# Kernel tuning notes

Hardware: AMD Instinct MI355X
Metric: run time of the kernel (lower is better)

Reference implementation:

```python
import jax, jax.numpy as jnp
import numpy as np

N = 100000   # nodes
E = 1600000  # edges
F_IN = 128
HID = 128
C = 40
EPS = 1e-5


def setup_inputs() -> dict:
    key = jax.random.key(0)
    ks = jax.random.split(key, 8)
    x = jax.random.normal(ks[0], (N, F_IN), dtype=jnp.float32)
    edge_index = jax.random.randint(ks[1], (2, E), 0, N, dtype=jnp.int32)
    s = 0.05
    return {
        "x": x,
        "edge_index": edge_index,
        "W1": jax.random.normal(ks[2], (F_IN, HID), dtype=jnp.float32) * s,
        "b1": jnp.zeros((HID,), jnp.float32),
        "g1": jnp.ones((HID,), jnp.float32),
        "be1": jnp.zeros((HID,), jnp.float32),
        "W2": jax.random.normal(ks[3], (HID, HID), dtype=jnp.float32) * s,
        "b2": jnp.zeros((HID,), jnp.float32),
        "g2": jnp.ones((HID,), jnp.float32),
        "be2": jnp.zeros((HID,), jnp.float32),
        "W3": jax.random.normal(ks[4], (HID, C), dtype=jnp.float32) * s,
        "b3": jnp.zeros((C,), jnp.float32),
    }


def _gcn_conv(x, W, b, src, dst, deg_inv_sqrt):
    # h = X W; then symmetric-normalized aggregation over edges (incl. self loops)
    h = x @ W                                  # [N, out]
    coef = deg_inv_sqrt[src] * deg_inv_sqrt[dst]  # [E+N]
    msg = h[src] * coef[:, None]               # gather + scale
    out = jax.ops.segment_sum(msg, dst, num_segments=N)
    return out + b


def _batchnorm(x, g, be):
    mean = jnp.mean(x, axis=0)
    var = jnp.mean(jnp.square(x - mean), axis=0)  # biased var (torch BN train)
    return (x - mean) * jax.lax.rsqrt(var + EPS) * g + be


def reference(x, edge_index, W1, b1, g1, be1, W2, b2, g2, be2, W3, b3):
    # add self loops once
    loop = jnp.arange(N, dtype=edge_index.dtype)
    src = jnp.concatenate([edge_index[0], loop])
    dst = jnp.concatenate([edge_index[1], loop])
    deg = jax.ops.segment_sum(jnp.ones_like(dst, dtype=x.dtype), dst, num_segments=N)
    dinv = jax.lax.rsqrt(deg)  # deg >= 1 due to self loops

    h = _gcn_conv(x, W1, b1, src, dst, dinv)
    h = _batchnorm(h, g1, be1)
    h = h + x                      # residual: hidden_dim == num_features
    h = jax.nn.relu(h)             # dropout: eval-mode identity

    h = _gcn_conv(h, W2, b2, src, dst, dinv)
    h = _batchnorm(h, g2, be2)
    h = jax.nn.relu(h)

    h = _gcn_conv(h, W3, b3, src, dst, dinv)
    return jax.nn.log_softmax(h, axis=1)
```

## Files before the change

### kernel.cpp

```cpp
#include <hip/hip_runtime.h>
#include <hip/hip_bf16.h>

#define NN 100000
#define EE 1600000
#define HID 128
#define CLS 40
#define EPSBN 1e-5f
#define NBUK ((NN + 255) >> 8)
#define CAP 6144
#define EPB 4096
#define GROWS (NN / 8)
#define FINB 500

typedef float f32x4 __attribute__((ext_vector_type(4)));
typedef float f32x2 __attribute__((ext_vector_type(2)));
typedef short s16x8 __attribute__((ext_vector_type(8)));
union U48 { uint4 u; s16x8 s; };

static __device__ __forceinline__ unsigned short f2bf(float f) {
    unsigned u = __float_as_uint(f);
    unsigned r = (u + 0x7fff + ((u >> 16) & 1)) >> 16;
    return (unsigned short)r;
}
static __device__ __forceinline__ unsigned pack2(float a, float b) {
    return (unsigned)f2bf(a) | ((unsigned)f2bf(b) << 16);
}
static __device__ __forceinline__ float bflo(unsigned v) { return __uint_as_float(v << 16); }
static __device__ __forceinline__ float bfhi(unsigned v) { return __uint_as_float(v & 0xffff0000u); }


__global__ void prep_all(const float* __restrict__ W1, const float* __restrict__ W2,
                         const float* __restrict__ W3,
                         unsigned* __restrict__ Wf1, unsigned* __restrict__ Wf2,
                         unsigned* __restrict__ Wf3,
                         int* gcur, float* stats1, float* stats2) {
    int blk = blockIdx.x;
    int tid = threadIdx.x;
    if (blk < 64) {
        const float* W = (blk < 32) ? W1 : W2;
        unsigned* Wf = (blk < 32) ? Wf1 : Wf2;
        int t = ((blk & 31) << 8) + tid;
        int q = t & 3, lane = (t >> 2) & 63, f = t >> 8;
        int ks = f >> 3, ct = f & 7;
        int k = ks * 32 + ((lane >> 4) << 3) + q * 2;
        int col = ct * 16 + (lane & 15);
        Wf[t] = pack2(W[k * 128 + col], W[(k + 1) * 128 + col]);
    } else if (blk < 76) {
        int t = ((blk - 64) << 8) + tid;
        int q = t & 3, lane = (t >> 2) & 63, f = t >> 8;
        int ks = f / 3, ct = f - ks * 3;
        int k = ks * 32 + ((lane >> 4) << 3) + q * 2;
        int col = ct * 16 + (lane & 15);
        float v0 = (col < CLS) ? W3[k * CLS + col] : 0.0f;
        float v1 = (col < CLS) ? W3[(k + 1) * CLS + col] : 0.0f;
        Wf3[t] = pack2(v0, v1);
    } else {
        int j = ((blk - 76) << 8) + tid;
        if (j < NBUK) gcur[j] = j * CAP;
        if (blk == 76) {
            stats1[tid] = 0.0f;
            stats2[tid] = 0.0f;
        }
    }
}


__global__ __launch_bounds__(256) void fill_p1_binned(const int* __restrict__ src,
                                                      const int* __restrict__ dst,
                                                      int* gcur, int* __restrict__ tmp) {
    __shared__ int cnt[NBUK];
    __shared__ int base[NBUK];
    int tid = threadIdx.x;
    for (int j = tid; j < NBUK; j += 256) cnt[j] = 0;
    __syncthreads();

    int es[16], ed[16];
    int i0 = blockIdx.x * EPB;
#pragma unroll
    for (int k = 0; k < 16; k++) {
        int i = i0 + k * 256 + tid;
        bool ok = i < EE;
        es[k] = ok ? src[i] : -1;
        ed[k] = ok ? dst[i] : 0;
        if (ok) atomicAdd(&cnt[ed[k] >> 8], 1);
    }
    __syncthreads();
    for (int j = tid; j < NBUK; j += 256) {
        int c = cnt[j];
        base[j] = c ? atomicAdd(&gcur[j], c) : 0;
        cnt[j] = 0;
    }
    __syncthreads();
#pragma unroll
    for (int k = 0; k < 16; k++) {
        if (es[k] >= 0) {
            int b = ed[k] >> 8;
            int r = atomicAdd(&cnt[b], 1);
            tmp[base[b] + r] = (es[k] << 8) | (ed[k] & 255);
        }
    }
}

__global__ __launch_bounds__(512) void bucket_scan(const int* __restrict__ gcur,
                                                   int* __restrict__ gbase,
                                                   int* __restrict__ row_ptr) {
    __shared__ int sc[512];
    int tid = threadIdx.x;
    int v = (tid < NBUK) ? gcur[tid] - tid * CAP : 0;
    sc[tid] = v;
    __syncthreads();
    for (int off = 1; off < 512; off <<= 1) {
        int t = (tid >= off) ? sc[tid - off] : 0;
        __syncthreads();
        sc[tid] += t;
        __syncthreads();
    }
    if (tid < NBUK) gbase[tid] = sc[tid] - v;
    if (tid == NBUK - 1) {
        gbase[NBUK] = sc[tid];
        row_ptr[NN] = sc[tid];
    }
}

__global__ __launch_bounds__(256) void fill_p2(const int* __restrict__ tmp,
                                               const int* __restrict__ gcur,
                                               const int* __restrict__ gbase,
                                               float* __restrict__ dinv,
                                               int* __restrict__ row_ptr,
                                               int* __restrict__ csr) {
    __shared__ int cnt[256];
    __shared__ int sc[256];
    __shared__ int cur[256];
    int b = blockIdx.x;
    int tid = threadIdx.x;
    int total = gcur[b] - b * CAP;
    cnt[tid] = 0;
    __syncthreads();
    int lo = b * CAP;
    for (int k = tid; k < total; k += 256) atomicAdd(&cnt[tmp[lo + k] & 255], 1);
    __syncthreads();
    int c = cnt[tid];
    sc[tid] = c;
    __syncthreads();
    for (int off = 1; off < 256; off <<= 1) {
        int t = (tid >= off) ? sc[tid - off] : 0;
        __syncthreads();
        sc[tid] += t;
        __syncthreads();
    }
    int node = (b << 8) + tid;
    int rp = gbase[b] + sc[tid] - c;
    if (node < NN) {
        dinv[node] = rsqrtf((float)(c + 1));
        row_ptr[node] = rp;
    }
    cur[tid] = rp;
    __syncthreads();
    for (int k = tid; k < total; k += 256) {
        int v = tmp[lo + k];
        int p = atomicAdd(&cur[v & 255], 1);
        csr[p] = ((unsigned)v) >> 8;
    }
}


#define LDA 136

template <int MODE>
__global__ __launch_bounds__(256) void gemm128_mfma(const float* __restrict__ Xf,
                                                    const unsigned* __restrict__ Xb,
                                                    const unsigned* __restrict__ Wf,
                                                    const float* __restrict__ stats,
                                                    const float* __restrict__ gam,
                                                    const float* __restrict__ bet,
                                                    const float* __restrict__ xres,
                                                    const float* __restrict__ dinv,
                                                    unsigned char* __restrict__ Hb) {
    __shared__ unsigned short As[64 * LDA];
    __shared__ float scs[128];
    __shared__ float shs[128];
    int t = threadIdx.x;
    int lane = t & 63, w = t >> 6;
    int wr = w >> 1, wc = w & 1;
    int blk_row = blockIdx.x * 64;
    const float invN = 1.0f / (float)NN;

    s16x8 b[4][4];
    const uint4* Wv = (const uint4*)Wf;
#pragma unroll
    for (int ks = 0; ks < 4; ks++)
#pragma unroll
        for (int ct = 0; ct < 4; ct++) {
            int f = ks * 8 + wc * 4 + ct;
            U48 u; u.u = Wv[f * 64 + lane];
            b[ks][ct] = u.s;
        }

    if (MODE == 1) {
        if (t < 128) {
            float mean = stats[t] * invN;
            float var = stats[128 + t] * invN - mean * mean;
            float sc = gam[t] * rsqrtf(var + EPSBN);
            scs[t] = sc;
            shs[t] = bet[t] - mean * sc;
        }
        __syncthreads();
        const uint2* H2 = (const uint2*)Xb;
        const float4* R4 = (const float4*)xres;
#pragma unroll
        for (int i = 0; i < 8; i++) {
            int idx = i * 256 + t;
            int row = idx >> 5, c4 = idx & 31;
            int grow = blk_row + row;
            uint2 h = make_uint2(0u, 0u);
            float4 r = make_float4(0, 0, 0, 0);
            if (grow < NN) {
                h = H2[(size_t)grow * 32 + c4];
                r = R4[(size_t)grow * 32 + c4];
            }
            int f0 = c4 * 4;
            float v0 = fmaxf(fmaf(bflo(h.x), scs[f0 + 0], shs[f0 + 0]) + r.x, 0.0f);
            float v1 = fmaxf(fmaf(bfhi(h.x), scs[f0 + 1], shs[f0 + 1]) + r.y, 0.0f);
            float v2 = fmaxf(fmaf(bflo(h.y), scs[f0 + 2], shs[f0 + 2]) + r.z, 0.0f);
            float v3 = fmaxf(fmaf(bfhi(h.y), scs[f0 + 3], shs[f0 + 3]) + r.w, 0.0f);
            *(uint2*)&As[row * LDA + c4 * 4] = make_uint2(pack2(v0, v1), pack2(v2, v3));
        }
    } else {
        const float4* X4 = (const float4*)Xf;
#pragma unroll
        for (int i = 0; i < 8; i++) {
            int idx = i * 256 + t;
            int row = idx >> 5, c4 = idx & 31;
            int grow = blk_row + row;
            float4 a = make_float4(0, 0, 0, 0);
            if (grow < NN) a = X4[(size_t)grow * 32 + c4];
            *(uint2*)&As[row * LDA + c4 * 4] = make_uint2(pack2(a.x, a.y), pack2(a.z, a.w));
        }
    }
    __syncthreads();

    f32x4 acc[2][4] = {};
    int lrow = lane & 15;
    int koff = (lane >> 4) << 3;

#pragma unroll
    for (int ks = 0; ks < 4; ks++) {
        int k0 = ks * 32 + koff;
#pragma unroll
        for (int rf = 0; rf < 2; rf++) {
            int rloc = wr * 32 + rf * 16 + lrow;
            U48 a;
            a.u = *(const uint4*)&As[rloc * LDA + k0];
#pragma unroll
            for (int ct = 0; ct < 4; ct++)
                acc[rf][ct] = __builtin_amdgcn_mfma_f32_16x16x32_bf16(a.s, b[ks][ct], acc[rf][ct], 0, 0, 0);
        }
    }

#pragma unroll
    for (int rf = 0; rf < 2; rf++) {
        int rbase = blk_row + wr * 32 + rf * 16 + ((lane >> 4) << 2);
        float dv[4];
#pragma unroll
        for (int r = 0; r < 4; r++) dv[r] = (rbase + r < NN) ? dinv[rbase + r] : 0.0f;
#pragma unroll
        for (int ct = 0; ct < 4; ct++) {
            int col = wc * 64 + ct * 16 + lrow;
#pragma unroll
            for (int r = 0; r < 4; r++) {
                int row = rbase + r;
                if (row < NN) {
                    int pv = __builtin_amdgcn_cvt_pk_fp8_f32(acc[rf][ct][r] * dv[r], 0.0f, 0, false);
                    Hb[(size_t)row * 128 + col] = (unsigned char)pv;
                }
            }
        }
    }
}

__global__ __launch_bounds__(256) void gemm40_mfma(const unsigned* __restrict__ Xb,
                                                   const unsigned* __restrict__ Wf,
                                                   const float* __restrict__ stats,
                                                   const float* __restrict__ gam,
                                                   const float* __restrict__ bet,
                                                   const float* __restrict__ dinv,
                                                   unsigned char* __restrict__ H3) {
    __shared__ unsigned short As[64 * LDA];
    __shared__ float scs[128];
    __shared__ float shs[128];
    int t = threadIdx.x;
    int lane = t & 63, w = t >> 6;
    int blk_row = blockIdx.x * 64;
    const float invN = 1.0f / (float)NN;

    s16x8 b[4][3];
    const uint4* Wv = (const uint4*)Wf;
#pragma unroll
    for (int ks = 0; ks < 4; ks++)
#pragma unroll
        for (int ct = 0; ct < 3; ct++) {
            U48 u; u.u = Wv[(ks * 3 + ct) * 64 + lane];
            b[ks][ct] = u.s;
        }

    if (t < 128) {
        float mean = stats[t] * invN;
        float var = stats[128 + t] * invN - mean * mean;
        float sc = gam[t] * rsqrtf(var + EPSBN);
        scs[t] = sc;
        shs[t] = bet[t] - mean * sc;
    }
    __syncthreads();
    const uint2* H2 = (const uint2*)Xb;
#pragma unroll
    for (int i = 0; i < 8; i++) {
        int idx = i * 256 + t;
        int row = idx >> 5, c4 = idx & 31;
        int grow = blk_row + row;
        uint2 h = make_uint2(0u, 0u);
        if (grow < NN) h = H2[(size_t)grow * 32 + c4];
        int f0 = c4 * 4;
        float v0 = fmaxf(fmaf(bflo(h.x), scs[f0 + 0], shs[f0 + 0]), 0.0f);
        float v1 = fmaxf(fmaf(bfhi(h.x), scs[f0 + 1], shs[f0 + 1]), 0.0f);
        float v2 = fmaxf(fmaf(bflo(h.y), scs[f0 + 2], shs[f0 + 2]), 0.0f);
        float v3 = fmaxf(fmaf(bfhi(h.y), scs[f0 + 3], shs[f0 + 3]), 0.0f);
        *(uint2*)&As[row * LDA + c4 * 4] = make_uint2(pack2(v0, v1), pack2(v2, v3));
    }
    __syncthreads();

    f32x4 acc[3] = {};
    int lrow = lane & 15;
    int koff = (lane >> 4) << 3;

#pragma unroll
    for (int ks = 0; ks < 4; ks++) {
        int k0 = ks * 32 + koff;
        int rloc = w * 16 + lrow;
        U48 a;
        a.u = *(const uint4*)&As[rloc * LDA + k0];
#pragma unroll
        for (int ct = 0; ct < 3; ct++)
            acc[ct] = __builtin_amdgcn_mfma_f32_16x16x32_bf16(a.s, b[ks][ct], acc[ct], 0, 0, 0);
    }

    int rbase = blk_row + w * 16 + ((lane >> 4) << 2);
    float dv[4];
#pragma unroll
    for (int r = 0; r < 4; r++) dv[r] = (rbase + r < NN) ? dinv[rbase + r] : 0.0f;
#pragma unroll
    for (int ct = 0; ct < 3; ct++) {
        int col = ct * 16 + lrow;
        if (col >= CLS) continue;
#pragma unroll
        for (int r = 0; r < 4; r++) {
            int row = rbase + r;
            if (row < NN) {
                int pv = __builtin_amdgcn_cvt_pk_fp8_f32(acc[ct][r] * dv[r], 0.0f, 0, false);
                H3[(size_t)row * CLS + col] = (unsigned char)pv;
            }
        }
    }
}


__global__ __launch_bounds__(256) void agg128_half(const unsigned* __restrict__ h8,
                                                   const int* __restrict__ row_ptr,
                                                   const int* __restrict__ csr,
                                                   const float* __restrict__ dinv,
                                                   const float* __restrict__ bias,
                                                   uint2* __restrict__ outb,
                                                   float* __restrict__ gpart) {
    __shared__ float red[4][256];
    int tid = threadIdx.x;
    int wid = tid >> 6;
    int lane = tid & 63;
    int half = lane >> 5, l = lane & 31;
    int node = blockIdx.x * 8 + wid * 2 + half;

    unsigned sv = h8[(size_t)node * 32 + l];
    f32x2 alo = __builtin_amdgcn_cvt_pk_f32_fp8(sv, false);
    f32x2 ahi = __builtin_amdgcn_cvt_pk_f32_fp8(sv, true);

    int beg = row_ptr[node], end = row_ptr[node + 1];
    int cnt = end - beg;
    int cmax = max(cnt, __shfl_xor(cnt, 32));
    int hb = (lane & 32);

    for (int k = 0; k < cmax; k += 12) {
        int bidx = beg + k + l;
        int cl = (bidx < end) ? bidx : beg;
        int myv = (l < 12) ? csr[cl] : 0;
        unsigned g[12];
#pragma unroll
        for (int j = 0; j < 12; j++) {
            int si = __shfl(myv, hb + j);
            int idx = beg + k + j;
            g[j] = (idx < end) ? h8[(size_t)si * 32 + l] : 0u;
        }
#pragma unroll
        for (int j = 0; j < 12; j++) {
            alo += __builtin_amdgcn_cvt_pk_f32_fp8(g[j], false);
            ahi += __builtin_amdgcn_cvt_pk_f32_fp8(g[j], true);
        }
    }

    float di = dinv[node];
    float4 b = *(const float4*)&bias[l * 4];
    float o0 = fmaf(alo.x, di, b.x), o1 = fmaf(alo.y, di, b.y);
    float o2 = fmaf(ahi.x, di, b.z), o3 = fmaf(ahi.y, di, b.w);
    outb[(size_t)node * 32 + l] = make_uint2(pack2(o0, o1), pack2(o2, o3));

    float s0 = o0, s1 = o1, s2 = o2, s3 = o3;
    float q0 = o0 * o0, q1 = o1 * o1, q2 = o2 * o2, q3 = o3 * o3;
    s0 += __shfl_xor(s0, 32); s1 += __shfl_xor(s1, 32);
    s2 += __shfl_xor(s2, 32); s3 += __shfl_xor(s3, 32);
    q0 += __shfl_xor(q0, 32); q1 += __shfl_xor(q1, 32);
    q2 += __shfl_xor(q2, 32); q3 += __shfl_xor(q3, 32);
    if (half == 0) {
        red[wid][l * 4 + 0] = s0; red[wid][l * 4 + 1] = s1;
        red[wid][l * 4 + 2] = s2; red[wid][l * 4 + 3] = s3;
        red[wid][128 + l * 4 + 0] = q0; red[wid][128 + l * 4 + 1] = q1;
        red[wid][128 + l * 4 + 2] = q2; red[wid][128 + l * 4 + 3] = q3;
    }
    __syncthreads();
    float pv = red[0][tid] + red[1][tid] + red[2][tid] + red[3][tid];
    gpart[(size_t)blockIdx.x * 256 + tid] = pv;
}

__global__ __launch_bounds__(256) void agg40_lsm(const unsigned* __restrict__ h3,
                                                 const int* __restrict__ row_ptr,
                                                 const int* __restrict__ csr,
                                                 const float* __restrict__ dinv,
                                                 const float* __restrict__ b3,
                                                 float* __restrict__ out) {
    int wid = threadIdx.x >> 6;
    int lane = threadIdx.x & 63;
    int half = lane >> 5, l30 = lane & 31;
    int slot = l30 / 10;
    int fp = l30 - slot * 10;
    bool sok = slot < 3;
    int node = blockIdx.x * 8 + wid * 2 + half;

    f32x2 alo = {0.0f, 0.0f}, ahi = {0.0f, 0.0f};
    if (slot == 0) {
        unsigned v = h3[(size_t)node * 10 + fp];
        alo = __builtin_amdgcn_cvt_pk_f32_fp8(v, false);
        ahi = __builtin_amdgcn_cvt_pk_f32_fp8(v, true);
    }
    int beg = row_ptr[node], end = row_ptr[node + 1];
    int cnt = end - beg;
    for (int k = 0; k < cnt; k += 12) {
#pragma unroll
        for (int jj = 0; jj < 4; jj++) {
            int idx = beg + k + jj * 3 + slot;
            bool on = sok && (idx < end);
            int s = csr[on ? idx : beg];
            unsigned g = on ? h3[(size_t)s * 10 + fp] : 0u;
            alo += __builtin_amdgcn_cvt_pk_f32_fp8(g, false);
            ahi += __builtin_amdgcn_cvt_pk_f32_fp8(g, true);
        }
    }
    float a0 = alo.x, a1 = alo.y, a2 = ahi.x, a3 = ahi.y;
    float t0 = __shfl(a0, lane + 10), t1 = __shfl(a1, lane + 10);
    float t2 = __shfl(a2, lane + 10), t3 = __shfl(a3, lane + 10);
    float u0 = __shfl(a0, lane + 20), u1 = __shfl(a1, lane + 20);
    float u2 = __shfl(a2, lane + 20), u3 = __shfl(a3, lane + 20);
    bool fin = l30 < 10;
    float l0 = 0.0f, l1 = 0.0f, l2 = 0.0f, l3 = 0.0f;
    if (fin) {
        float di = dinv[node];
        float4 b = *(const float4*)&b3[fp * 4];
        l0 = fmaf(a0 + t0 + u0, di, b.x);
        l1 = fmaf(a1 + t1 + u1, di, b.y);
        l2 = fmaf(a2 + t2 + u2, di, b.z);
        l3 = fmaf(a3 + t3 + u3, di, b.w);
    }
    float m = fin ? fmaxf(fmaxf(l0, l1), fmaxf(l2, l3)) : -1e30f;
#pragma unroll
    for (int off = 16; off > 0; off >>= 1) m = fmaxf(m, __shfl_xor(m, off));
    float s = fin ? (expf(l0 - m) + expf(l1 - m) + expf(l2 - m) + expf(l3 - m)) : 0.0f;
#pragma unroll
    for (int off = 16; off > 0; off >>= 1) s += __shfl_xor(s, off);
    float lse = m + logf(s);
    if (fin)
        *(float4*)&out[(size_t)node * CLS + fp * 4] =
            make_float4(l0 - lse, l1 - lse, l2 - lse, l3 - lse);
}


__global__ __launch_bounds__(256) void bn_final(const float* __restrict__ gpart,
                                                float* __restrict__ stats) {
    int t = threadIdx.x;
    int k0 = blockIdx.x * 25;
    float s = 0.0f;
#pragma unroll 5
    for (int k = k0; k < k0 + 25; k++)
        s += gpart[(size_t)k * 256 + t];
    atomicAdd(&stats[t], s);
}


extern "C" void kernel_launch(void* const* d_in, const int* in_sizes, int n_in,
                              void* d_out, int out_size, void* d_ws, size_t ws_size,
                              hipStream_t stream) {
    const float* x   = (const float*)d_in[0];
    const int*   ei  = (const int*)d_in[1];
    const float* W1  = (const float*)d_in[2];
    const float* b1  = (const float*)d_in[3];
    const float* g1  = (const float*)d_in[4];
    const float* be1 = (const float*)d_in[5];
    const float* W2  = (const float*)d_in[6];
    const float* b2  = (const float*)d_in[7];
    const float* g2  = (const float*)d_in[8];
    const float* be2 = (const float*)d_in[9];
    const float* W3  = (const float*)d_in[10];
    const float* b3  = (const float*)d_in[11];
    float* out = (float*)d_out;

    const int* src = ei;
    const int* dst = ei + EE;

    char* w = (char*)d_ws;
    size_t off = 0;
    auto alloc = [&](size_t bytes) {
        void* p = w + off;
        off += (bytes + 255) & ~(size_t)255;
        return p;
    };
    float* dinv      = (float*)alloc((size_t)NN * 4);
    int*   row_ptr   = (int*)alloc((size_t)(NN + 1) * 4);
    int*   gcur      = (int*)alloc((size_t)NBUK * 4);
    int*   gbase     = (int*)alloc((size_t)(NBUK + 1) * 4);
    int*   tmp       = (int*)alloc((size_t)NBUK * CAP * 4);
    int*   csr       = (int*)alloc((size_t)EE * 4);
    float* stats1    = (float*)alloc(256 * 4);
    float* stats2    = (float*)alloc(256 * 4);
    float* gpart     = (float*)alloc((size_t)GROWS * 256 * 4);
    unsigned* Wf1    = (unsigned*)alloc(8192 * 4);
    unsigned* Wf2    = (unsigned*)alloc(8192 * 4);
    unsigned* Wf3    = (unsigned*)alloc(3072 * 4);
    unsigned* aH     = (unsigned*)alloc((size_t)NN * 64 * 4);
    unsigned char* hB8 = (unsigned char*)alloc((size_t)NN * 128);
    unsigned char* h3b = (unsigned char*)alloc((size_t)NN * 40);

    const int NB_P1 = (EE + EPB - 1) / EPB;
    const int NB_G  = (NN + 63) / 64;

    prep_all<<<78, 256, 0, stream>>>(W1, W2, W3, Wf1, Wf2, Wf3, gcur, stats1, stats2);
    fill_p1_binned<<<NB_P1, 256, 0, stream>>>(src, dst, gcur, tmp);
    bucket_scan<<<1, 512, 0, stream>>>(gcur, gbase, row_ptr);
    fill_p2<<<NBUK, 256, 0, stream>>>(tmp, gcur, gbase, dinv, row_ptr, csr);

    gemm128_mfma<0><<<NB_G, 256, 0, stream>>>(x, nullptr, Wf1, nullptr, nullptr, nullptr, nullptr, dinv, hB8);
    agg128_half<<<NN / 8, 256, 0, stream>>>((const unsigned*)hB8, row_ptr, csr, dinv, b1, (uint2*)aH, gpart);
    bn_final<<<FINB, 256, 0, stream>>>(gpart, stats1);

    gemm128_mfma<1><<<NB_G, 256, 0, stream>>>(nullptr, aH, Wf2, stats1, g1, be1, x, dinv, hB8);
    agg128_half<<<NN / 8, 256, 0, stream>>>((const unsigned*)hB8, row_ptr, csr, dinv, b2, (uint2*)aH, gpart);
    bn_final<<<FINB, 256, 0, stream>>>(gpart, stats2);

    gemm40_mfma<<<NB_G, 256, 0, stream>>>(aH, Wf3, stats2, g2, be2, dinv, h3b);
    agg40_lsm<<<NN / 8, 256, 0, stream>>>((const unsigned*)h3b, row_ptr, csr, dinv, b3, out);
}
```

Measured before the change: 264.0 us.

## Pre-cast x to bf16 once and shuffle-broadcast CSR indices in final aggregation

A new kernel converts the fp32 input x to packed bf16 once, so both GEMM passes read half-size data: layer 1's input load and layer 2's residual read. This adds a separate launch that reads x in fp32 and writes a bf16 copy, and it rounds the residual to bf16, which costs some precision. In the 40-class aggregation, each group of 12 lanes now loads the CSR neighbor indices once and broadcasts them with shuffles, replacing redundant per-lane index loads.

```diff
diff --git a/kernel.cpp b/kernel.cpp
--- a/kernel.cpp
+++ b/kernel.cpp
@@ -64,6 +64,15 @@
     }
 }
 
+__global__ __launch_bounds__(256) void xcast(const float2* __restrict__ x,
+                                             unsigned* __restrict__ xb) {
+    int i = blockIdx.x * 256 + threadIdx.x;
+    if (i < NN * 64) {
+        float2 v = x[i];
+        xb[i] = pack2(v.x, v.y);
+    }
+}
+
 
 __global__ __launch_bounds__(256) void fill_p1_binned(const int* __restrict__ src,
                                                       const int* __restrict__ dst,
@@ -167,13 +176,12 @@
 #define LDA 136
 
 template <int MODE>
-__global__ __launch_bounds__(256) void gemm128_mfma(const float* __restrict__ Xf,
-                                                    const unsigned* __restrict__ Xb,
+__global__ __launch_bounds__(256) void gemm128_mfma(const unsigned* __restrict__ Xb,
                                                     const unsigned* __restrict__ Wf,
                                                     const float* __restrict__ stats,
                                                     const float* __restrict__ gam,
                                                     const float* __restrict__ bet,
-                                                    const float* __restrict__ xres,
+                                                    const unsigned* __restrict__ xres,
                                                     const float* __restrict__ dinv,
                                                     unsigned char* __restrict__ Hb) {
     __shared__ unsigned short As[64 * LDA];
@@ -206,35 +214,35 @@
         }
         __syncthreads();
         const uint2* H2 = (const uint2*)Xb;
-        const float4* R4 = (const float4*)xres;
+        const uint2* R2 = (const uint2*)xres;
 #pragma unroll
         for (int i = 0; i < 8; i++) {
             int idx = i * 256 + t;
             int row = idx >> 5, c4 = idx & 31;
             int grow = blk_row + row;
             uint2 h = make_uint2(0u, 0u);
-            float4 r = make_float4(0, 0, 0, 0);
+            uint2 rr = make_uint2(0u, 0u);
             if (grow < NN) {
                 h = H2[(size_t)grow * 32 + c4];
-                r = R4[(size_t)grow * 32 + c4];
+                rr = R2[(size_t)grow * 32 + c4];
             }
             int f0 = c4 * 4;
-            float v0 = fmaxf(fmaf(bflo(h.x), scs[f0 + 0], shs[f0 + 0]) + r.x, 0.0f);
-            float v1 = fmaxf(fmaf(bfhi(h.x), scs[f0 + 1], shs[f0 + 1]) + r.y, 0.0f);
-            float v2 = fmaxf(fmaf(bflo(h.y), scs[f0 + 2], shs[f0 + 2]) + r.z, 0.0f);
-            float v3 = fmaxf(fmaf(bfhi(h.y), scs[f0 + 3], shs[f0 + 3]) + r.w, 0.0f);
+            float v0 = fmaxf(fmaf(bflo(h.x), scs[f0 + 0], shs[f0 + 0]) + bflo(rr.x), 0.0f);
+            float v1 = fmaxf(fmaf(bfhi(h.x), scs[f0 + 1], shs[f0 + 1]) + bfhi(rr.x), 0.0f);
+            float v2 = fmaxf(fmaf(bflo(h.y), scs[f0 + 2], shs[f0 + 2]) + bflo(rr.y), 0.0f);
+            float v3 = fmaxf(fmaf(bfhi(h.y), scs[f0 + 3], shs[f0 + 3]) + bfhi(rr.y), 0.0f);
             *(uint2*)&As[row * LDA + c4 * 4] = make_uint2(pack2(v0, v1), pack2(v2, v3));
         }
     } else {
-        const float4* X4 = (const float4*)Xf;
-#pragma unroll
-        for (int i = 0; i < 8; i++) {
+        const uint4* X4 = (const uint4*)Xb;
+#pragma unroll
+        for (int i = 0; i < 4; i++) {
             int idx = i * 256 + t;
-            int row = idx >> 5, c4 = idx & 31;
+            int row = idx >> 4, c8 = idx & 15;
             int grow = blk_row + row;
-            float4 a = make_float4(0, 0, 0, 0);
-            if (grow < NN) a = X4[(size_t)grow * 32 + c4];
-            *(uint2*)&As[row * LDA + c4 * 4] = make_uint2(pack2(a.x, a.y), pack2(a.z, a.w));
+            uint4 a = make_uint4(0u, 0u, 0u, 0u);
+            if (grow < NN) a = X4[(size_t)grow * 16 + c8];
+            *(uint4*)&As[row * LDA + c8 * 8] = a;
         }
     }
     __syncthreads();
@@ -440,6 +448,7 @@
     int fp = l30 - slot * 10;
     bool sok = slot < 3;
     int node = blockIdx.x * 8 + wid * 2 + half;
+    int hb = (lane & 32);
 
     f32x2 alo = {0.0f, 0.0f}, ahi = {0.0f, 0.0f};
     if (slot == 0) {
@@ -450,12 +459,16 @@
     int beg = row_ptr[node], end = row_ptr[node + 1];
     int cnt = end - beg;
     for (int k = 0; k < cnt; k += 12) {
+        int bidx = beg + k + l30;
+        int cl = (bidx < end) ? bidx : beg;
+        int myv = (l30 < 12) ? csr[cl] : 0;
 #pragma unroll
         for (int jj = 0; jj < 4; jj++) {
-            int idx = beg + k + jj * 3 + slot;
+            int e = jj * 3 + slot;
+            int si = __shfl(myv, hb + e);
+            int idx = beg + k + e;
             bool on = sok && (idx < end);
-            int s = csr[on ? idx : beg];
-            unsigned g = on ? h3[(size_t)s * 10 + fp] : 0u;
+            unsigned g = on ? h3[(size_t)si * 10 + fp] : 0u;
             alo += __builtin_amdgcn_cvt_pk_f32_fp8(g, false);
             ahi += __builtin_amdgcn_cvt_pk_f32_fp8(g, true);
         }
@@ -539,23 +552,26 @@
     unsigned* Wf1    = (unsigned*)alloc(8192 * 4);
     unsigned* Wf2    = (unsigned*)alloc(8192 * 4);
     unsigned* Wf3    = (unsigned*)alloc(3072 * 4);
+    unsigned* xb     = (unsigned*)alloc((size_t)NN * 64 * 4);
     unsigned* aH     = (unsigned*)alloc((size_t)NN * 64 * 4);
     unsigned char* hB8 = (unsigned char*)alloc((size_t)NN * 128);
     unsigned char* h3b = (unsigned char*)alloc((size_t)NN * 40);
 
     const int NB_P1 = (EE + EPB - 1) / EPB;
     const int NB_G  = (NN + 63) / 64;
+    const int NB_X  = (NN * 64 + 255) / 256;
 
     prep_all<<<78, 256, 0, stream>>>(W1, W2, W3, Wf1, Wf2, Wf3, gcur, stats1, stats2);
+    xcast<<<NB_X, 256, 0, stream>>>((const float2*)x, xb);
     fill_p1_binned<<<NB_P1, 256, 0, stream>>>(src, dst, gcur, tmp);
     bucket_scan<<<1, 512, 0, stream>>>(gcur, gbase, row_ptr);
     fill_p2<<<NBUK, 256, 0, stream>>>(tmp, gcur, gbase, dinv, row_ptr, csr);
 
-    gemm128_mfma<0><<<NB_G, 256, 0, stream>>>(x, nullptr, Wf1, nullptr, nullptr, nullptr, nullptr, dinv, hB8);
+    gemm128_mfma<0><<<NB_G, 256, 0, stream>>>(xb, Wf1, nullptr, nullptr, nullptr, nullptr, dinv, hB8);
     agg128_half<<<NN / 8, 256, 0, stream>>>((const unsigned*)hB8, row_ptr, csr, dinv, b1, (uint2*)aH, gpart);
     bn_final<<<FINB, 256, 0, stream>>>(gpart, stats1);
 
-    gemm128_mfma<1><<<NB_G, 256, 0, stream>>>(nullptr, aH, Wf2, stats1, g1, be1, x, dinv, hB8);
+    gemm128_mfma<1><<<NB_G, 256, 0, stream>>>(aH, Wf2, stats1, g1, be1, xb, dinv, hB8);
     agg128_half<<<NN / 8, 256, 0, stream>>>((const unsigned*)hB8, row_ptr, csr, dinv, b2, (uint2*)aH, gpart);
     bn_final<<<FINB, 256, 0, stream>>>(gpart, stats2);
 
```

Measured after the change: 265.0 us. No clear change (+0.4%).
